# Optimization experiments

Hardware: AMD Instinct MI355X
Metric: run time of the kernel (lower is better)

The kernel has to match this reference:

```python
import jax, jax.numpy as jnp
import numpy as np

N_NODES = 100000
N_EDGES = 3200000
DIM = 16


def setup_inputs() -> dict:
    key = jax.random.key(0)
    k1, k2, k3, k4 = jax.random.split(key, 4)
    state_input = jax.random.normal(k1, (N_NODES, DIM), dtype=jnp.float32)
    row = jax.random.randint(k2, (N_EDGES,), 0, N_NODES, dtype=jnp.int32)
    col = jax.random.randint(k3, (N_EDGES,), 0, N_NODES, dtype=jnp.int32)
    edge_weights = jax.random.uniform(k4, (N_EDGES,), dtype=jnp.float32)
    return {"state_input": state_input, "row": row, "col": col,
            "edge_weights": edge_weights}


def reference(state_input, row, col, edge_weights):
    # f_eq: per-dim self dynamics, f(x) = -x  -> [N, dim]
    self_diff = -state_input

    # gather pair endpoints: x_1 = state[col], x_2 = state[row]
    # g_eq: sin(x_2 - x_1) per dim (Kuramoto-style coupling) -> [E, dim]
    neighbor_processed = jnp.sin(state_input[row] - state_input[col])

    # weight by edge weight and scatter-sum into destination nodes (col)
    aggregated_sum = jax.ops.segment_sum(
        neighbor_processed * edge_weights[:, None], col,
        num_segments=state_input.shape[0])  # [N, dim]

    # s_eq: elementwise tanh on aggregated sum
    interact_diff = jnp.tanh(aggregated_sum)

    return (self_diff + interact_diff,
            (state_input, self_diff),
            (aggregated_sum, interact_diff))
```

## Files before the change

kernel.cpp:

```cpp
#include <hip/hip_runtime.h>
#include <hip/hip_fp16.h>
#include <math.h>

#define N_NODES 100000
#define N_EDGES 3200000
#define DIM 16
#define NSZ (N_NODES * DIM)

#define NPB 128
#define NBUCK 782
#define NBLK 512
#define EPB 6256
#define CAP 4864
#define PRK 5

typedef float nvec4 __attribute__((ext_vector_type(4)));

__global__ __launch_bounds__(512)
void hist_table(const float* __restrict__ state, __half* __restrict__ hs,
                const int* __restrict__ col, unsigned* __restrict__ tbl,
                int* __restrict__ totals) {
    __shared__ int hcnt[NBUCK];
    int t = threadIdx.x, blk = blockIdx.x;
    for (int j = t; j < NBUCK; j += 512) hcnt[j] = 0;
    for (int i = blk * 512 + t; i < NSZ / 4; i += NBLK * 512) {
        nvec4 v = __builtin_nontemporal_load(&((const nvec4*)state)[i]);
        union { __half2 h[2]; float2 f; } u;
        u.h[0] = __floats2half2_rn(v.x, v.y);
        u.h[1] = __floats2half2_rn(v.z, v.w);
        ((float2*)hs)[i] = u.f;
    }
    __syncthreads();
    int e0 = blk * EPB;
    int eN = e0 + EPB; if (eN > N_EDGES) eN = N_EDGES;
    int nch = (eN - e0) >> 2;
    const int4* c4p = (const int4*)(col + e0);
    for (int i = t; i < nch; i += 512) {
        int4 c = c4p[i];
        atomicAdd(&hcnt[c.x >> 7], 1);
        atomicAdd(&hcnt[c.y >> 7], 1);
        atomicAdd(&hcnt[c.z >> 7], 1);
        atomicAdd(&hcnt[c.w >> 7], 1);
    }
    __syncthreads();
    for (int j = t; j < NBUCK; j += 512) {
        int c = hcnt[j];
        tbl[(size_t)j * NBLK + blk] = (unsigned)c;
        if (c) atomicAdd(&totals[j], c);
    }
}

__global__ __launch_bounds__(1024)
void scan_off(const int* __restrict__ totals, int* __restrict__ off) {
    __shared__ int wsum[16];
    int t = threadIdx.x;
    int i0 = 2 * t, i1 = 2 * t + 1;
    int v0 = (i0 < NBUCK) ? totals[i0] : 0;
    int v1 = (i1 < NBUCK) ? totals[i1] : 0;
    int p = v0 + v1, ps = p;
    #pragma unroll
    for (int d = 1; d < 64; d <<= 1) {
        int u = __shfl_up(ps, d, 64);
        if ((t & 63) >= d) ps += u;
    }
    if ((t & 63) == 63) wsum[t >> 6] = ps;
    __syncthreads();
    int wid = t >> 6, wbase = 0;
    #pragma unroll
    for (int k = 0; k < 16; ++k) wbase += (k < wid) ? wsum[k] : 0;
    int ex = wbase + ps - p;
    if (i0 < NBUCK) off[i0 + 1] = ex + v0;
    if (i1 < NBUCK) off[i1 + 1] = ex + v0 + v1;
    if (t == 0) off[0] = 0;
}

__global__ __launch_bounds__(512)
void base_scan(unsigned* __restrict__ tbl, const int* __restrict__ off) {
    __shared__ int wsum[8];
    int b = blockIdx.x, t = threadIdx.x;
    int v = (int)tbl[(size_t)b * NBLK + t];
    int ps = v;
    #pragma unroll
    for (int d = 1; d < 64; d <<= 1) {
        int u = __shfl_up(ps, d, 64);
        if ((t & 63) >= d) ps += u;
    }
    if ((t & 63) == 63) wsum[t >> 6] = ps;
    __syncthreads();
    int wid = t >> 6, wbase = 0;
    #pragma unroll
    for (int k = 0; k < 8; ++k) wbase += (k < wid) ? wsum[k] : 0;
    tbl[(size_t)b * NBLK + t] = (unsigned)(off[b] + wbase + ps - v);
}

__global__ __launch_bounds__(512)
void sort_write(const int* __restrict__ row, const int* __restrict__ col,
                const float* __restrict__ w, const unsigned* __restrict__ tbl,
                const int* __restrict__ off,
                unsigned long long* __restrict__ packed) {
    __shared__ unsigned long long sbuf[EPB];
    __shared__ int sc[1024];
    __shared__ int cur[NBUCK];
    __shared__ int gbase[NBUCK];
    __shared__ int wsum[8];
    int t = threadIdx.x, blk = blockIdx.x;
    int e0 = blk * EPB;
    int eN = e0 + EPB; if (eN > N_EDGES) eN = N_EDGES;
    int cnt = eN - e0;

    for (int j = t; j < NBUCK; j += 512) {
        int b0 = (int)tbl[(size_t)j * NBLK + blk];
        int b1 = (blk == NBLK - 1) ? off[j + 1]
                                   : (int)tbl[(size_t)j * NBLK + blk + 1];
        gbase[j] = b0;
        cur[j] = b1 - b0;
    }
    __syncthreads();
    {
        int i0 = 2 * t, i1 = 2 * t + 1;
        int v0 = (i0 < NBUCK) ? cur[i0] : 0;
        int v1 = (i1 < NBUCK) ? cur[i1] : 0;
        int p = v0 + v1, ps = p;
        #pragma unroll
        for (int d = 1; d < 64; d <<= 1) {
            int u = __shfl_up(ps, d, 64);
            if ((t & 63) >= d) ps += u;
        }
        if ((t & 63) == 63) wsum[t >> 6] = ps;
        __syncthreads();
        int wid = t >> 6, wbase = 0;
        #pragma unroll
        for (int k = 0; k < 8; ++k) wbase += (k < wid) ? wsum[k] : 0;
        int ex = wbase + ps - p;
        if (i0 < NBUCK) { sc[i0] = ex;      cur[i0] = ex; }
        if (i1 < NBUCK) { sc[i1] = ex + v0; cur[i1] = ex + v0; }
    }
    __syncthreads();
    {
        int nch = cnt >> 2;
        const int4*  c4p = (const int4*)(col + e0);
        const int4*  r4p = (const int4*)(row + e0);
        const float4* w4p = (const float4*)(w + e0);
        for (int i = t; i < nch; i += 512) {
            int4 c = c4p[i]; int4 r = r4p[i]; float4 ww = w4p[i];
            int pos;
            pos = atomicAdd(&cur[c.x >> 7], 1);
            sbuf[pos] = ((unsigned long long)(unsigned)c.x << 47)
                      | ((unsigned long long)(unsigned)r.x << 30)
                      | (unsigned long long)(__float_as_uint(ww.x) >> 2);
            pos = atomicAdd(&cur[c.y >> 7], 1);
            sbuf[pos] = ((unsigned long long)(unsigned)c.y << 47)
                      | ((unsigned long long)(unsigned)r.y << 30)
                      | (unsigned long long)(__float_as_uint(ww.y) >> 2);
            pos = atomicAdd(&cur[c.z >> 7], 1);
            sbuf[pos] = ((unsigned long long)(unsigned)c.z << 47)
                      | ((unsigned long long)(unsigned)r.z << 30)
                      | (unsigned long long)(__float_as_uint(ww.z) >> 2);
            pos = atomicAdd(&cur[c.w >> 7], 1);
            sbuf[pos] = ((unsigned long long)(unsigned)c.w << 47)
                      | ((unsigned long long)(unsigned)r.w << 30)
                      | (unsigned long long)(__float_as_uint(ww.w) >> 2);
        }
    }
    __syncthreads();
    for (int i = t; i < cnt; i += 512) {
        unsigned long long pv = sbuf[i];
        int b = (int)(pv >> 54);
        __builtin_nontemporal_store(pv, &packed[gbase[b] + (i - sc[b])]);
    }
}

__device__ inline float4 edge_acc(float4 a, const float4 xx,
                                  unsigned long long p, float2 hbits) {
    union { float2 f; __half2 h[2]; } u; u.f = hbits;
    float2 lo = __half22float2(u.h[0]);
    float2 hi = __half22float2(u.h[1]);
    float we = __uint_as_float(((unsigned)p & 0x3FFFFFFFu) << 2);
    a.x += __sinf(lo.x - xx.x) * we;
    a.y += __sinf(lo.y - xx.y) * we;
    a.z += __sinf(hi.x - xx.z) * we;
    a.w += __sinf(hi.y - xx.w) * we;
    return a;
}

__global__ __launch_bounds__(1024, 8)
void bucket_sort_aggregate(const float* __restrict__ state,
                           const __half2* __restrict__ hs2,
                           const int* __restrict__ off,
                           const unsigned long long* __restrict__ packed,
                           float* __restrict__ out) {
    __shared__ unsigned long long sbuf[CAP];
    __shared__ int s_cnt[NPB], s_start[NPB], s_cur[NPB];
    __shared__ int s_wsum;
    int b = blockIdx.x, t = threadIdx.x;
    int q = t & 3, sub = (t >> 2) & 1, g = t >> 3;
    int beg = off[b], end = off[b + 1];

    int n = b * NPB + g;
    bool valid = (n < N_NODES);
    float4 xx = valid ? ((const float4*)state)[n * 4 + q]
                      : make_float4(0.f, 0.f, 0.f, 0.f);
    float4 acc = make_float4(0.f, 0.f, 0.f, 0.f);
    const float2* hsf2 = (const float2*)hs2;

    for (int tbeg = beg; tbeg < end; tbeg += CAP) {
        int tend = tbeg + CAP; if (tend > end) tend = end;
        if (t < NPB) s_cnt[t] = 0;
        __syncthreads();

        unsigned long long pr[PRK];
        #pragma unroll
        for (int k = 0; k < PRK; ++k) {
            int e = tbeg + t + k * 1024;
            if (e < tend) {
                pr[k] = __builtin_nontemporal_load(&packed[e]);
                atomicAdd(&s_cnt[(unsigned)(pr[k] >> 47) & 127u], 1);
            }
        }
        __syncthreads();

        {
            int v = (t < NPB) ? s_cnt[t] : 0;
            int ps = v;
            #pragma unroll
            for (int d = 1; d < 64; d <<= 1) {
                int u = __shfl_up(ps, d, 64);
                if ((t & 63) >= d) ps += u;
            }
            if (t == 63) s_wsum = ps;
            __syncthreads();
            if (t < NPB) {
                int ex = ps - v + ((t >= 64) ? s_wsum : 0);
                s_start[t] = ex;
                s_cur[t] = ex;
            }
        }
        __syncthreads();

        #pragma unroll
        for (int k = 0; k < PRK; ++k) {
            int e = tbeg + t + k * 1024;
            if (e < tend) {
                int cl = (int)((pr[k] >> 47) & 127u);
                int pos = atomicAdd(&s_cur[cl], 1);
                sbuf[pos] = pr[k];
            }
        }
        __syncthreads();

        {
            int es = s_start[g], ee = s_cur[g];
            float4 a = acc;
            int e = es + sub;
            for (; e + 6 < ee; e += 8) {
                unsigned long long p0 = sbuf[e];
                unsigned long long p1 = sbuf[e + 2];
                unsigned long long p2 = sbuf[e + 4];
                unsigned long long p3 = sbuf[e + 6];
                float2 h0 = hsf2[(unsigned)((p0 >> 30) & 0x1FFFFu) * 4u + q];
                float2 h1 = hsf2[(unsigned)((p1 >> 30) & 0x1FFFFu) * 4u + q];
                float2 h2 = hsf2[(unsigned)((p2 >> 30) & 0x1FFFFu) * 4u + q];
                float2 h3 = hsf2[(unsigned)((p3 >> 30) & 0x1FFFFu) * 4u + q];
                a = edge_acc(a, xx, p0, h0);
                a = edge_acc(a, xx, p1, h1);
                a = edge_acc(a, xx, p2, h2);
                a = edge_acc(a, xx, p3, h3);
            }
            for (; e < ee; e += 2) {
                unsigned long long p0 = sbuf[e];
                float2 h0 = hsf2[(unsigned)((p0 >> 30) & 0x1FFFFu) * 4u + q];
                a = edge_acc(a, xx, p0, h0);
            }
            acc = a;
        }
        __syncthreads();
    }

    acc.x += __shfl_xor(acc.x, 4, 64);
    acc.y += __shfl_xor(acc.y, 4, 64);
    acc.z += __shfl_xor(acc.z, 4, 64);
    acc.w += __shfl_xor(acc.w, 4, 64);

    if (valid) {
        float4 th = make_float4(tanhf(acc.x), tanhf(acc.y),
                                tanhf(acc.z), tanhf(acc.w));
        int gdx = n * 4 + q;
        if (sub == 0) {
            ((float4*)(out + 0 * (size_t)NSZ))[gdx] =
                make_float4(th.x - xx.x, th.y - xx.y, th.z - xx.z, th.w - xx.w);
            ((float4*)(out + 2 * (size_t)NSZ))[gdx] =
                make_float4(-xx.x, -xx.y, -xx.z, -xx.w);
            ((float4*)(out + 4 * (size_t)NSZ))[gdx] = th;
        } else {
            ((float4*)(out + 1 * (size_t)NSZ))[gdx] = xx;
            ((float4*)(out + 3 * (size_t)NSZ))[gdx] = acc;
        }
    }
}

__global__ __launch_bounds__(256)
void edge_kernel(const float* __restrict__ state, const int* __restrict__ row,
                 const int* __restrict__ col, const float* __restrict__ w,
                 float* __restrict__ agg) {
    int idx = blockIdx.x * blockDim.x + threadIdx.x;
    if (idx >= N_EDGES * 4) return;
    int e = idx >> 2, qq = idx & 3;
    int r = row[e], c = col[e];
    float we = w[e];
    const float4 xr = ((const float4*)state)[r * 4 + qq];
    const float4 xcv = ((const float4*)state)[c * 4 + qq];
    float* dst = agg + c * DIM + qq * 4;
    atomicAdd(dst + 0, sinf(xr.x - xcv.x) * we);
    atomicAdd(dst + 1, sinf(xr.y - xcv.y) * we);
    atomicAdd(dst + 2, sinf(xr.z - xcv.z) * we);
    atomicAdd(dst + 3, sinf(xr.w - xcv.w) * we);
}

__global__ __launch_bounds__(256)
void node_kernel(const float* __restrict__ state, const float* __restrict__ agg,
                 float* __restrict__ out) {
    int idx = blockIdx.x * blockDim.x + threadIdx.x;
    if (idx >= N_NODES * 4) return;
    float4 x = ((const float4*)state)[idx];
    float4 a = ((const float4*)agg)[idx];
    float4 tv = make_float4(tanhf(a.x), tanhf(a.y), tanhf(a.z), tanhf(a.w));
    ((float4*)(out + 0 * NSZ))[idx] = make_float4(tv.x - x.x, tv.y - x.y,
                                                  tv.z - x.z, tv.w - x.w);
    ((float4*)(out + 1 * NSZ))[idx] = x;
    ((float4*)(out + 2 * NSZ))[idx] = make_float4(-x.x, -x.y, -x.z, -x.w);
    ((float4*)(out + 4 * NSZ))[idx] = tv;
}

extern "C" void kernel_launch(void* const* d_in, const int* in_sizes, int n_in,
                              void* d_out, int out_size, void* d_ws, size_t ws_size,
                              hipStream_t stream) {
    const float* state = (const float*)d_in[0];
    const int*   row   = (const int*)d_in[1];
    const int*   col   = (const int*)d_in[2];
    const float* w     = (const float*)d_in[3];
    float* out = (float*)d_out;

    size_t packed_off = 0;
    size_t half_off   = packed_off + (size_t)N_EDGES * 8;
    size_t tbl_off    = half_off + (size_t)NSZ * 2;
    size_t tot_off    = tbl_off + (size_t)NBUCK * NBLK * 4;
    size_t off_off    = tot_off + (size_t)NBUCK * 4;
    size_t needed     = off_off + (size_t)(NBUCK + 1) * 4;

    if (ws_size >= needed) {
        unsigned long long* packed =
            (unsigned long long*)((char*)d_ws + packed_off);
        __half* hs    = (__half*)((char*)d_ws + half_off);
        unsigned* tbl = (unsigned*)((char*)d_ws + tbl_off);
        int* totals   = (int*)((char*)d_ws + tot_off);
        int* off      = (int*)((char*)d_ws + off_off);

        (void)hipMemsetAsync(totals, 0, (size_t)NBUCK * sizeof(int), stream);
        hist_table<<<NBLK, 512, 0, stream>>>(state, hs, col, tbl, totals);
        scan_off<<<1, 1024, 0, stream>>>(totals, off);
        base_scan<<<NBUCK, 512, 0, stream>>>(tbl, off);
        sort_write<<<NBLK, 512, 0, stream>>>(row, col, w, tbl, off, packed);
        bucket_sort_aggregate<<<NBUCK, 1024, 0, stream>>>(
            state, (const __half2*)hs, off, packed, out);
    } else {
        float* agg = out + 3 * NSZ;
        (void)hipMemsetAsync(agg, 0, NSZ * sizeof(float), stream);
        edge_kernel<<<(N_EDGES * 4 + 255) / 256, 256, 0, stream>>>(
            state, row, col, w, agg);
        node_kernel<<<(N_NODES * 4 + 255) / 256, 256, 0, stream>>>(
            state, agg, out);
    }
}
```

Measured before the change: 185.5 us.

## Use sin/cos angle-difference identity, global-atomic scatter, and smaller node buckets

```diff
diff --git a/kernel.cpp b/kernel.cpp
--- a/kernel.cpp
+++ b/kernel.cpp
@@ -7,57 +7,61 @@
 #define DIM 16
 #define NSZ (N_NODES * DIM)
 
-#define NPB 128
-#define NBUCK 782
-#define NBLK 512
-#define EPB 6256
-#define CAP 4864
-#define PRK 5
+#define NPB 32
+#define NBUCK 3125
+#define CAP 1536
+#define PRK 3
 
 typedef float nvec4 __attribute__((ext_vector_type(4)));
 
 __global__ __launch_bounds__(512)
-void hist_table(const float* __restrict__ state, __half* __restrict__ hs,
-                const int* __restrict__ col, unsigned* __restrict__ tbl,
-                int* __restrict__ totals) {
+void prep(const float* __restrict__ state, const int* __restrict__ col,
+          float* __restrict__ scp, float* __restrict__ out,
+          int* __restrict__ totals) {
     __shared__ int hcnt[NBUCK];
-    int t = threadIdx.x, blk = blockIdx.x;
+    int t = threadIdx.x;
+    int gid = blockIdx.x * 512 + t;
+    int gsz = gridDim.x * 512;
     for (int j = t; j < NBUCK; j += 512) hcnt[j] = 0;
-    for (int i = blk * 512 + t; i < NSZ / 4; i += NBLK * 512) {
+    for (int i = gid; i < NSZ / 4; i += gsz) {
         nvec4 v = __builtin_nontemporal_load(&((const nvec4*)state)[i]);
-        union { __half2 h[2]; float2 f; } u;
-        u.h[0] = __floats2half2_rn(v.x, v.y);
-        u.h[1] = __floats2half2_rn(v.z, v.w);
-        ((float2*)hs)[i] = u.f;
+        union { __half2 h[4]; nvec4 f; } u;
+        u.h[0] = __floats2half2_rn(__sinf(v.x), __cosf(v.x));
+        u.h[1] = __floats2half2_rn(__sinf(v.y), __cosf(v.y));
+        u.h[2] = __floats2half2_rn(__sinf(v.z), __cosf(v.z));
+        u.h[3] = __floats2half2_rn(__sinf(v.w), __cosf(v.w));
+        ((nvec4*)scp)[i] = u.f;
+        __builtin_nontemporal_store(v, &((nvec4*)(out + 1 * (size_t)NSZ))[i]);
+        nvec4 nv = {-v.x, -v.y, -v.z, -v.w};
+        __builtin_nontemporal_store(nv, &((nvec4*)(out + 2 * (size_t)NSZ))[i]);
     }
     __syncthreads();
-    int e0 = blk * EPB;
-    int eN = e0 + EPB; if (eN > N_EDGES) eN = N_EDGES;
-    int nch = (eN - e0) >> 2;
-    const int4* c4p = (const int4*)(col + e0);
-    for (int i = t; i < nch; i += 512) {
-        int4 c = c4p[i];
-        atomicAdd(&hcnt[c.x >> 7], 1);
-        atomicAdd(&hcnt[c.y >> 7], 1);
-        atomicAdd(&hcnt[c.z >> 7], 1);
-        atomicAdd(&hcnt[c.w >> 7], 1);
+    for (int i = gid; i < N_EDGES / 4; i += gsz) {
+        int4 c = ((const int4*)col)[i];
+        atomicAdd(&hcnt[c.x >> 5], 1);
+        atomicAdd(&hcnt[c.y >> 5], 1);
+        atomicAdd(&hcnt[c.z >> 5], 1);
+        atomicAdd(&hcnt[c.w >> 5], 1);
     }
     __syncthreads();
     for (int j = t; j < NBUCK; j += 512) {
         int c = hcnt[j];
-        tbl[(size_t)j * NBLK + blk] = (unsigned)c;
         if (c) atomicAdd(&totals[j], c);
     }
 }
 
 __global__ __launch_bounds__(1024)
-void scan_off(const int* __restrict__ totals, int* __restrict__ off) {
+void scan_off(const int* __restrict__ totals, int* __restrict__ off,
+              int* __restrict__ gcur) {
     __shared__ int wsum[16];
     int t = threadIdx.x;
-    int i0 = 2 * t, i1 = 2 * t + 1;
-    int v0 = (i0 < NBUCK) ? totals[i0] : 0;
-    int v1 = (i1 < NBUCK) ? totals[i1] : 0;
-    int p = v0 + v1, ps = p;
+    int base = t * 4;
+    int v0 = (base + 0 < NBUCK) ? totals[base + 0] : 0;
+    int v1 = (base + 1 < NBUCK) ? totals[base + 1] : 0;
+    int v2 = (base + 2 < NBUCK) ? totals[base + 2] : 0;
+    int v3 = (base + 3 < NBUCK) ? totals[base + 3] : 0;
+    int s = v0 + v1 + v2 + v3;
+    int ps = s;
     #pragma unroll
     for (int d = 1; d < 64; d <<= 1) {
         int u = __shfl_up(ps, d, 64);
@@ -68,140 +72,77 @@
     int wid = t >> 6, wbase = 0;
     #pragma unroll
     for (int k = 0; k < 16; ++k) wbase += (k < wid) ? wsum[k] : 0;
-    int ex = wbase + ps - p;
-    if (i0 < NBUCK) off[i0 + 1] = ex + v0;
-    if (i1 < NBUCK) off[i1 + 1] = ex + v0 + v1;
-    if (t == 0) off[0] = 0;
-}
-
-__global__ __launch_bounds__(512)
-void base_scan(unsigned* __restrict__ tbl, const int* __restrict__ off) {
-    __shared__ int wsum[8];
+    int o0 = wbase + ps - s;
+    int o1 = o0 + v0, o2 = o1 + v1, o3 = o2 + v2;
+    if (base     <= NBUCK) off[base]     = o0;
+    if (base + 1 <= NBUCK) off[base + 1] = o1;
+    if (base + 2 <= NBUCK) off[base + 2] = o2;
+    if (base + 3 <= NBUCK) off[base + 3] = o3;
+    if (base     < NBUCK) gcur[base]     = o0;
+    if (base + 1 < NBUCK) gcur[base + 1] = o1;
+    if (base + 2 < NBUCK) gcur[base + 2] = o2;
+    if (base + 3 < NBUCK) gcur[base + 3] = o3;
+}
+
+__global__ __launch_bounds__(256)
+void scatter(const int* __restrict__ row, const int* __restrict__ col,
+             const float* __restrict__ w, int* __restrict__ gcur,
+             unsigned long long* __restrict__ packed) {
+    int gid = blockIdx.x * 256 + threadIdx.x;
+    int gsz = gridDim.x * 256;
+    for (int i = gid; i < N_EDGES / 4; i += gsz) {
+        int4 c = ((const int4*)col)[i];
+        int4 r = ((const int4*)row)[i];
+        float4 ww = ((const float4*)w)[i];
+        int pos;
+        pos = atomicAdd(&gcur[c.x >> 5], 1);
+        packed[pos] = ((unsigned long long)(unsigned)c.x << 47)
+                    | ((unsigned long long)(unsigned)r.x << 30)
+                    | (unsigned long long)(__float_as_uint(ww.x) >> 2);
+        pos = atomicAdd(&gcur[c.y >> 5], 1);
+        packed[pos] = ((unsigned long long)(unsigned)c.y << 47)
+                    | ((unsigned long long)(unsigned)r.y << 30)
+                    | (unsigned long long)(__float_as_uint(ww.y) >> 2);
+        pos = atomicAdd(&gcur[c.z >> 5], 1);
+        packed[pos] = ((unsigned long long)(unsigned)c.z << 47)
+                    | ((unsigned long long)(unsigned)r.z << 30)
+                    | (unsigned long long)(__float_as_uint(ww.z) >> 2);
+        pos = atomicAdd(&gcur[c.w >> 5], 1);
+        packed[pos] = ((unsigned long long)(unsigned)c.w << 47)
+                    | ((unsigned long long)(unsigned)r.w << 30)
+                    | (unsigned long long)(__float_as_uint(ww.w) >> 2);
+    }
+}
+
+__device__ inline void acc_sc(float4& S, float4& C, unsigned long long p,
+                              nvec4 h) {
+    float we = __uint_as_float(((unsigned)p & 0x3FFFFFFFu) << 2);
+    union { nvec4 f; __half2 h2[4]; } uu; uu.f = h;
+    float2 f0 = __half22float2(uu.h2[0]);
+    float2 f1 = __half22float2(uu.h2[1]);
+    float2 f2 = __half22float2(uu.h2[2]);
+    float2 f3 = __half22float2(uu.h2[3]);
+    S.x += we * f0.x; C.x += we * f0.y;
+    S.y += we * f1.x; C.y += we * f1.y;
+    S.z += we * f2.x; C.z += we * f2.y;
+    S.w += we * f3.x; C.w += we * f3.y;
+}
+
+__global__ __launch_bounds__(512, 8)
+void aggregate(const float* __restrict__ state, const float* __restrict__ scp,
+               const int* __restrict__ off,
+               const unsigned long long* __restrict__ packed,
+               float* __restrict__ out) {
+    __shared__ unsigned long long sbuf[CAP];
+    __shared__ nvec4 stage[3 * NPB * 4];
+    __shared__ int s_cnt[NPB], s_start[NPB], s_cur[NPB];
     int b = blockIdx.x, t = threadIdx.x;
-    int v = (int)tbl[(size_t)b * NBLK + t];
-    int ps = v;
-    #pragma unroll
-    for (int d = 1; d < 64; d <<= 1) {
-        int u = __shfl_up(ps, d, 64);
-        if ((t & 63) >= d) ps += u;
-    }
-    if ((t & 63) == 63) wsum[t >> 6] = ps;
-    __syncthreads();
-    int wid = t >> 6, wbase = 0;
-    #pragma unroll
-    for (int k = 0; k < 8; ++k) wbase += (k < wid) ? wsum[k] : 0;
-    tbl[(size_t)b * NBLK + t] = (unsigned)(off[b] + wbase + ps - v);
-}
-
-__global__ __launch_bounds__(512)
-void sort_write(const int* __restrict__ row, const int* __restrict__ col,
-                const float* __restrict__ w, const unsigned* __restrict__ tbl,
-                const int* __restrict__ off,
-                unsigned long long* __restrict__ packed) {
-    __shared__ unsigned long long sbuf[EPB];
-    __shared__ int sc[1024];
-    __shared__ int cur[NBUCK];
-    __shared__ int gbase[NBUCK];
-    __shared__ int wsum[8];
-    int t = threadIdx.x, blk = blockIdx.x;
-    int e0 = blk * EPB;
-    int eN = e0 + EPB; if (eN > N_EDGES) eN = N_EDGES;
-    int cnt = eN - e0;
-
-    for (int j = t; j < NBUCK; j += 512) {
-        int b0 = (int)tbl[(size_t)j * NBLK + blk];
-        int b1 = (blk == NBLK - 1) ? off[j + 1]
-                                   : (int)tbl[(size_t)j * NBLK + blk + 1];
-        gbase[j] = b0;
-        cur[j] = b1 - b0;
-    }
-    __syncthreads();
-    {
-        int i0 = 2 * t, i1 = 2 * t + 1;
-        int v0 = (i0 < NBUCK) ? cur[i0] : 0;
-        int v1 = (i1 < NBUCK) ? cur[i1] : 0;
-        int p = v0 + v1, ps = p;
-        #pragma unroll
-        for (int d = 1; d < 64; d <<= 1) {
-            int u = __shfl_up(ps, d, 64);
-            if ((t & 63) >= d) ps += u;
-        }
-        if ((t & 63) == 63) wsum[t >> 6] = ps;
-        __syncthreads();
-        int wid = t >> 6, wbase = 0;
-        #pragma unroll
-        for (int k = 0; k < 8; ++k) wbase += (k < wid) ? wsum[k] : 0;
-        int ex = wbase + ps - p;
-        if (i0 < NBUCK) { sc[i0] = ex;      cur[i0] = ex; }
-        if (i1 < NBUCK) { sc[i1] = ex + v0; cur[i1] = ex + v0; }
-    }
-    __syncthreads();
-    {
-        int nch = cnt >> 2;
-        const int4*  c4p = (const int4*)(col + e0);
-        const int4*  r4p = (const int4*)(row + e0);
-        const float4* w4p = (const float4*)(w + e0);
-        for (int i = t; i < nch; i += 512) {
-            int4 c = c4p[i]; int4 r = r4p[i]; float4 ww = w4p[i];
-            int pos;
-            pos = atomicAdd(&cur[c.x >> 7], 1);
-            sbuf[pos] = ((unsigned long long)(unsigned)c.x << 47)
-                      | ((unsigned long long)(unsigned)r.x << 30)
-                      | (unsigned long long)(__float_as_uint(ww.x) >> 2);
-            pos = atomicAdd(&cur[c.y >> 7], 1);
-            sbuf[pos] = ((unsigned long long)(unsigned)c.y << 47)
-                      | ((unsigned long long)(unsigned)r.y << 30)
-                      | (unsigned long long)(__float_as_uint(ww.y) >> 2);
-            pos = atomicAdd(&cur[c.z >> 7], 1);
-            sbuf[pos] = ((unsigned long long)(unsigned)c.z << 47)
-                      | ((unsigned long long)(unsigned)r.z << 30)
-                      | (unsigned long long)(__float_as_uint(ww.z) >> 2);
-            pos = atomicAdd(&cur[c.w >> 7], 1);
-            sbuf[pos] = ((unsigned long long)(unsigned)c.w << 47)
-                      | ((unsigned long long)(unsigned)r.w << 30)
-                      | (unsigned long long)(__float_as_uint(ww.w) >> 2);
-        }
-    }
-    __syncthreads();
-    for (int i = t; i < cnt; i += 512) {
-        unsigned long long pv = sbuf[i];
-        int b = (int)(pv >> 54);
-        __builtin_nontemporal_store(pv, &packed[gbase[b] + (i - sc[b])]);
-    }
-}
-
-__device__ inline float4 edge_acc(float4 a, const float4 xx,
-                                  unsigned long long p, float2 hbits) {
-    union { float2 f; __half2 h[2]; } u; u.f = hbits;
-    float2 lo = __half22float2(u.h[0]);
-    float2 hi = __half22float2(u.h[1]);
-    float we = __uint_as_float(((unsigned)p & 0x3FFFFFFFu) << 2);
-    a.x += __sinf(lo.x - xx.x) * we;
-    a.y += __sinf(lo.y - xx.y) * we;
-    a.z += __sinf(hi.x - xx.z) * we;
-    a.w += __sinf(hi.y - xx.w) * we;
-    return a;
-}
-
-__global__ __launch_bounds__(1024, 8)
-void bucket_sort_aggregate(const float* __restrict__ state,
-                           const __half2* __restrict__ hs2,
-                           const int* __restrict__ off,
-                           const unsigned long long* __restrict__ packed,
-                           float* __restrict__ out) {
-    __shared__ unsigned long long sbuf[CAP];
-    __shared__ int s_cnt[NPB], s_start[NPB], s_cur[NPB];
-    __shared__ int s_wsum;
-    int b = blockIdx.x, t = threadIdx.x;
-    int q = t & 3, sub = (t >> 2) & 1, g = t >> 3;
+    int q = t & 3, sub = (t >> 2) & 3, g = t >> 4;
     int beg = off[b], end = off[b + 1];
-
     int n = b * NPB + g;
-    bool valid = (n < N_NODES);
-    float4 xx = valid ? ((const float4*)state)[n * 4 + q]
-                      : make_float4(0.f, 0.f, 0.f, 0.f);
-    float4 acc = make_float4(0.f, 0.f, 0.f, 0.f);
-    const float2* hsf2 = (const float2*)hs2;
+    float4 xx = ((const float4*)state)[n * 4 + q];
+    float4 S = {0.f, 0.f, 0.f, 0.f}, C = {0.f, 0.f, 0.f, 0.f};
+    const nvec4* scp4 = (const nvec4*)scp;
 
     for (int tbeg = beg; tbeg < end; tbeg += CAP) {
         int tend = tbeg + CAP; if (tend > end) tend = end;
@@ -211,37 +152,31 @@
         unsigned long long pr[PRK];
         #pragma unroll
         for (int k = 0; k < PRK; ++k) {
-            int e = tbeg + t + k * 1024;
+            int e = tbeg + t + k * 512;
             if (e < tend) {
                 pr[k] = __builtin_nontemporal_load(&packed[e]);
-                atomicAdd(&s_cnt[(unsigned)(pr[k] >> 47) & 127u], 1);
+                atomicAdd(&s_cnt[(unsigned)(pr[k] >> 47) & 31u], 1);
             }
         }
         __syncthreads();
 
-        {
-            int v = (t < NPB) ? s_cnt[t] : 0;
-            int ps = v;
+        if (t < 32) {
+            int v = s_cnt[t], ps = v;
             #pragma unroll
-            for (int d = 1; d < 64; d <<= 1) {
-                int u = __shfl_up(ps, d, 64);
-                if ((t & 63) >= d) ps += u;
-            }
-            if (t == 63) s_wsum = ps;
-            __syncthreads();
-            if (t < NPB) {
-                int ex = ps - v + ((t >= 64) ? s_wsum : 0);
-                s_start[t] = ex;
-                s_cur[t] = ex;
-            }
+            for (int d = 1; d < 32; d <<= 1) {
+                int uu = __shfl_up(ps, d, 64);
+                if (t >= d) ps += uu;
+            }
+            s_start[t] = ps - v;
+            s_cur[t] = ps - v;
         }
         __syncthreads();
 
         #pragma unroll
         for (int k = 0; k < PRK; ++k) {
-            int e = tbeg + t + k * 1024;
+            int e = tbeg + t + k * 512;
             if (e < tend) {
-                int cl = (int)((pr[k] >> 47) & 127u);
+                int cl = (int)((pr[k] >> 47) & 31u);
                 int pos = atomicAdd(&s_cur[cl], 1);
                 sbuf[pos] = pr[k];
             }
@@ -250,51 +185,61 @@
 
         {
             int es = s_start[g], ee = s_cur[g];
-            float4 a = acc;
             int e = es + sub;
-            for (; e + 6 < ee; e += 8) {
+            for (; e + 12 < ee; e += 16) {
                 unsigned long long p0 = sbuf[e];
-                unsigned long long p1 = sbuf[e + 2];
-                unsigned long long p2 = sbuf[e + 4];
-                unsigned long long p3 = sbuf[e + 6];
-                float2 h0 = hsf2[(unsigned)((p0 >> 30) & 0x1FFFFu) * 4u + q];
-                float2 h1 = hsf2[(unsigned)((p1 >> 30) & 0x1FFFFu) * 4u + q];
-                float2 h2 = hsf2[(unsigned)((p2 >> 30) & 0x1FFFFu) * 4u + q];
-                float2 h3 = hsf2[(unsigned)((p3 >> 30) & 0x1FFFFu) * 4u + q];
-                a = edge_acc(a, xx, p0, h0);
-                a = edge_acc(a, xx, p1, h1);
-                a = edge_acc(a, xx, p2, h2);
-                a = edge_acc(a, xx, p3, h3);
-            }
-            for (; e < ee; e += 2) {
+                unsigned long long p1 = sbuf[e + 4];
+                unsigned long long p2 = sbuf[e + 8];
+                unsigned long long p3 = sbuf[e + 12];
+                nvec4 h0 = scp4[(unsigned)((p0 >> 30) & 0x1FFFFu) * 4u + q];
+                nvec4 h1 = scp4[(unsigned)((p1 >> 30) & 0x1FFFFu) * 4u + q];
+                nvec4 h2 = scp4[(unsigned)((p2 >> 30) & 0x1FFFFu) * 4u + q];
+                nvec4 h3 = scp4[(unsigned)((p3 >> 30) & 0x1FFFFu) * 4u + q];
+                acc_sc(S, C, p0, h0);
+                acc_sc(S, C, p1, h1);
+                acc_sc(S, C, p2, h2);
+                acc_sc(S, C, p3, h3);
+            }
+            for (; e < ee; e += 4) {
                 unsigned long long p0 = sbuf[e];
-                float2 h0 = hsf2[(unsigned)((p0 >> 30) & 0x1FFFFu) * 4u + q];
-                a = edge_acc(a, xx, p0, h0);
-            }
-            acc = a;
+                nvec4 h0 = scp4[(unsigned)((p0 >> 30) & 0x1FFFFu) * 4u + q];
+                acc_sc(S, C, p0, h0);
+            }
         }
         __syncthreads();
     }
 
-    acc.x += __shfl_xor(acc.x, 4, 64);
-    acc.y += __shfl_xor(acc.y, 4, 64);
-    acc.z += __shfl_xor(acc.z, 4, 64);
-    acc.w += __shfl_xor(acc.w, 4, 64);
-
-    if (valid) {
-        float4 th = make_float4(tanhf(acc.x), tanhf(acc.y),
-                                tanhf(acc.z), tanhf(acc.w));
-        int gdx = n * 4 + q;
-        if (sub == 0) {
-            ((float4*)(out + 0 * (size_t)NSZ))[gdx] =
-                make_float4(th.x - xx.x, th.y - xx.y, th.z - xx.z, th.w - xx.w);
-            ((float4*)(out + 2 * (size_t)NSZ))[gdx] =
-                make_float4(-xx.x, -xx.y, -xx.z, -xx.w);
-            ((float4*)(out + 4 * (size_t)NSZ))[gdx] = th;
-        } else {
-            ((float4*)(out + 1 * (size_t)NSZ))[gdx] = xx;
-            ((float4*)(out + 3 * (size_t)NSZ))[gdx] = acc;
-        }
+    S.x += __shfl_xor(S.x, 4, 64); S.y += __shfl_xor(S.y, 4, 64);
+    S.z += __shfl_xor(S.z, 4, 64); S.w += __shfl_xor(S.w, 4, 64);
+    C.x += __shfl_xor(C.x, 4, 64); C.y += __shfl_xor(C.y, 4, 64);
+    C.z += __shfl_xor(C.z, 4, 64); C.w += __shfl_xor(C.w, 4, 64);
+    S.x += __shfl_xor(S.x, 8, 64); S.y += __shfl_xor(S.y, 8, 64);
+    S.z += __shfl_xor(S.z, 8, 64); S.w += __shfl_xor(S.w, 8, 64);
+    C.x += __shfl_xor(C.x, 8, 64); C.y += __shfl_xor(C.y, 8, 64);
+    C.z += __shfl_xor(C.z, 8, 64); C.w += __shfl_xor(C.w, 8, 64);
+
+    if (sub == 0) {
+        float4 agg, th;
+        float sx, cx;
+        sx = __sinf(xx.x); cx = __cosf(xx.x); agg.x = cx * S.x - sx * C.x;
+        sx = __sinf(xx.y); cx = __cosf(xx.y); agg.y = cx * S.y - sx * C.y;
+        sx = __sinf(xx.z); cx = __cosf(xx.z); agg.z = cx * S.z - sx * C.z;
+        sx = __sinf(xx.w); cx = __cosf(xx.w); agg.w = cx * S.w - sx * C.w;
+        th.x = tanhf(agg.x); th.y = tanhf(agg.y);
+        th.z = tanhf(agg.z); th.w = tanhf(agg.w);
+        int slot = g * 4 + q;
+        stage[0 * 128 + slot] = (nvec4){th.x - xx.x, th.y - xx.y,
+                                        th.z - xx.z, th.w - xx.w};
+        stage[1 * 128 + slot] = (nvec4){agg.x, agg.y, agg.z, agg.w};
+        stage[2 * 128 + slot] = (nvec4){th.x, th.y, th.z, th.w};
+    }
+    __syncthreads();
+    if (t < 384) {
+        int a = t >> 7, j = t & 127;
+        nvec4 v = stage[t];
+        size_t arr = (a == 0) ? 0 : ((a == 1) ? 3 : 4);
+        __builtin_nontemporal_store(
+            v, &((nvec4*)(out + arr * (size_t)NSZ))[b * 128 + j]);
     }
 }
 
@@ -341,27 +286,25 @@
     float* out = (float*)d_out;
 
     size_t packed_off = 0;
-    size_t half_off   = packed_off + (size_t)N_EDGES * 8;
-    size_t tbl_off    = half_off + (size_t)NSZ * 2;
-    size_t tot_off    = tbl_off + (size_t)NBUCK * NBLK * 4;
-    size_t off_off    = tot_off + (size_t)NBUCK * 4;
-    size_t needed     = off_off + (size_t)(NBUCK + 1) * 4;
+    size_t scp_off    = packed_off + (size_t)N_EDGES * 8;
+    size_t tot_off    = scp_off + (size_t)NSZ * 4;
+    size_t off_off    = tot_off + ((size_t)NBUCK * 4 + 15) / 16 * 16;
+    size_t gcur_off   = off_off + ((size_t)(NBUCK + 1) * 4 + 15) / 16 * 16;
+    size_t needed     = gcur_off + (size_t)NBUCK * 4;
 
     if (ws_size >= needed) {
         unsigned long long* packed =
             (unsigned long long*)((char*)d_ws + packed_off);
-        __half* hs    = (__half*)((char*)d_ws + half_off);
-        unsigned* tbl = (unsigned*)((char*)d_ws + tbl_off);
-        int* totals   = (int*)((char*)d_ws + tot_off);
-        int* off      = (int*)((char*)d_ws + off_off);
+        float* scp  = (float*)((char*)d_ws + scp_off);
+        int* totals = (int*)((char*)d_ws + tot_off);
+        int* off    = (int*)((char*)d_ws + off_off);
+        int* gcur   = (int*)((char*)d_ws + gcur_off);
 
         (void)hipMemsetAsync(totals, 0, (size_t)NBUCK * sizeof(int), stream);
-        hist_table<<<NBLK, 512, 0, stream>>>(state, hs, col, tbl, totals);
-        scan_off<<<1, 1024, 0, stream>>>(totals, off);
-        base_scan<<<NBUCK, 512, 0, stream>>>(tbl, off);
-        sort_write<<<NBLK, 512, 0, stream>>>(row, col, w, tbl, off, packed);
-        bucket_sort_aggregate<<<NBUCK, 1024, 0, stream>>>(
-            state, (const __half2*)hs, off, packed, out);
+        prep<<<512, 512, 0, stream>>>(state, col, scp, out, totals);
+        scan_off<<<1, 1024, 0, stream>>>(totals, off, gcur);
+        scatter<<<1024, 256, 0, stream>>>(row, col, w, gcur, packed);
+        aggregate<<<NBUCK, 512, 0, stream>>>(state, scp, off, packed, out);
     } else {
         float* agg = out + 3 * NSZ;
         (void)hipMemsetAsync(agg, 0, NSZ * sizeof(float), stream);
```

Result: slower. 419.5 us (+126.2%).
